# Kernel optimization log

Hardware: AMD Instinct MI355X
Metric: run time of the kernel (lower is better)

Reference implementation:

```python
import jax, jax.numpy as jnp
import numpy as np

NUM_HEADS = 8
TAU = 0.5

@jax.custom_vjp
def spike(u):
    # Heaviside spike with rectangular surrogate gradient (width 1.0)
    return (u >= 0.0).astype(u.dtype)

def _spike_fwd(u):
    return spike(u), u

def _spike_bwd(u, g):
    return (g * (jnp.abs(u) < 0.5).astype(g.dtype),)

spike.defvjp(_spike_fwd, _spike_bwd)

def lif(x, thr=1.0):
    # Multi-step LIF over leading T axis: leaky integrate, fire, hard reset.
    def step(mem, xt):
        mem = mem * TAU + xt
        s = spike(mem - thr)
        return mem * (1.0 - s), s
    _, out = jax.lax.scan(step, jnp.zeros_like(x[0]), x)
    return out

def bn(x, g, b):
    # eval-mode BatchNorm over channel axis 2 (running_mean=0, running_var=1)
    shape = (1, 1, -1) + (1,) * (x.ndim - 3)
    return x * g.reshape(shape) + b.reshape(shape)

def ema_mems(q, alpha):
    # mems[0]=q[0]; mems[t]=alpha*mems[t-1]+(1-alpha)*q[t-1]
    def step(m, qp):
        m2 = alpha * m + (1.0 - alpha) * qp
        return m2, m2
    _, ms = jax.lax.scan(step, q[0], q[:-1])
    return jnp.concatenate([q[:1], ms], axis=0)

def setup_inputs() -> dict:
    key = jax.random.key(0)
    ks = jax.random.split(key, 16)
    T, B, C, H, W = 4, 16, 256, 32, 32
    Ch = 4 * C
    s = 0.05
    return {
        'x': jax.random.normal(ks[0], (T, B, C, H, W), jnp.float32),
        'q_w': jax.random.normal(ks[1], (C, C), jnp.float32) * s,
        'q_g': 1.0 + 0.02 * jax.random.normal(ks[2], (C,), jnp.float32),
        'q_b': 0.02 * jax.random.normal(ks[3], (C,), jnp.float32),
        'k_w': jax.random.normal(ks[4], (C, C), jnp.float32) * s,
        'k_g': 1.0 + 0.02 * jax.random.normal(ks[5], (C,), jnp.float32),
        'k_b': 0.02 * jax.random.normal(ks[6], (C,), jnp.float32),
        'proj_w': jax.random.normal(ks[7], (C, C), jnp.float32) * s,
        'proj_bias': 0.02 * jax.random.normal(ks[8], (C,), jnp.float32),
        'proj_g': 1.0 + 0.02 * jax.random.normal(ks[9], (C,), jnp.float32),
        'proj_b2': 0.02 * jax.random.normal(ks[10], (C,), jnp.float32),
        'mem_alpha': jnp.asarray(0.2, jnp.float32),
        'w1': jax.random.normal(ks[11], (Ch, C), jnp.float32) * s,
        'b1': 0.02 * jax.random.normal(ks[12], (Ch,), jnp.float32),
        'bn1_g': jnp.ones((Ch,), jnp.float32),
        'bn1_b': jnp.zeros((Ch,), jnp.float32),
        'w2': jax.random.normal(ks[13], (C, Ch), jnp.float32) * s,
        'b2': 0.02 * jax.random.normal(ks[14], (C,), jnp.float32),
        'bn2_g': jnp.ones((C,), jnp.float32),
        'bn2_b': jnp.zeros((C,), jnp.float32),
    }

def reference(x, q_w, q_g, q_b, k_w, k_g, k_b, proj_w, proj_bias, proj_g, proj_b2,
              mem_alpha, w1, b1, bn1_g, bn1_b, w2, b2, bn2_g, bn2_b):
    T, B, C, H, W = x.shape
    N = H * W
    h = NUM_HEADS
    d = C // h

    # ---- Token_QK_Attention ----
    xs = lif(x)                                   # [T,B,C,H,W] spikes
    xf = xs.reshape(T, B, C, N)
    q = lif(bn(jnp.einsum('tbcn,oc->tbon', xf, q_w), q_g, q_b))
    k = lif(bn(jnp.einsum('tbcn,oc->tbon', xf, k_w), k_g, k_b))
    q = q.reshape(T, B, h, d, N)
    k = k.reshape(T, B, h, d, N)
    mems = ema_mems(q, mem_alpha)                 # [T,B,h,d,N]
    # concat([mems,q], dim=3) then sum over dim 3 == sum(mems+q, dim 3)
    qsum = jnp.sum(mems + q, axis=3, keepdims=True)   # [T,B,h,1,N]
    attn = lif(qsum, thr=0.5)
    y = (attn * k).reshape(T, B, C, N)
    y = bn(jnp.einsum('tbcn,oc->tbon', y, proj_w) + proj_bias.reshape(1, 1, -1, 1),
           proj_g, proj_b2).reshape(T, B, C, H, W)
    x = x + y

    # ---- MLP (1x1 conv2d) ----
    z = lif(x)
    z = bn(jnp.einsum('tbchw,oc->tbohw', z, w1) + b1.reshape(1, 1, -1, 1, 1), bn1_g, bn1_b)
    z = lif(z)
    z = bn(jnp.einsum('tbchw,oc->tbohw', z, w2) + b2.reshape(1, 1, -1, 1, 1), bn2_g, bn2_b)
    return x + z
```

## Files before the change

### kernel.cpp

```cpp
#include <hip/hip_runtime.h>

typedef unsigned int u32;
typedef unsigned char u8;
typedef unsigned short u16;
typedef __attribute__((ext_vector_type(4))) u32 u32x4;
typedef __attribute__((ext_vector_type(4))) int i32x4;
typedef __attribute__((ext_vector_type(4))) float f32x4;

#define DEV __device__ __forceinline__

static constexpr size_t XS_OFF  = 0;
static constexpr size_t QS_OFF  = XS_OFF  + (size_t)16777216;
static constexpr size_t KS_OFF  = QS_OFF  + (size_t)16777216;
static constexpr size_t ATT_OFF = KS_OFF  + (size_t)16777216;
static constexpr size_t X2_OFF  = ATT_OFF + (size_t)1048576;
static constexpr size_t Z2_OFF  = X2_OFF  + (size_t)67108864;
static constexpr size_t WQK_OFF = Z2_OFF  + (size_t)67108864;
static constexpr size_t WP_OFF  = WQK_OFF + (size_t)524288;
static constexpr size_t W1_OFF  = WP_OFF  + (size_t)262144;
static constexpr size_t W2_OFF  = W1_OFF  + (size_t)1048576;
static constexpr size_t WS_NEED = W2_OFF  + (size_t)1048576;

DEV void gl_lds16(const void* gsrc, void* ldst){
  __builtin_amdgcn_global_load_lds(
      (const __attribute__((address_space(1))) unsigned int*)gsrc,
      (__attribute__((address_space(3))) unsigned int*)ldst, 16, 0, 0);
}

__global__ __launch_bounds__(256) void prep_all(
    const float* __restrict__ q_w, const float* __restrict__ k_w,
    const float* __restrict__ p_w, const float* __restrict__ w1,
    const float* __restrict__ w2,
    signed char* __restrict__ WQK, signed char* __restrict__ WP,
    signed char* __restrict__ W1p, signed char* __restrict__ W2p)
{
  const int bb = blockIdx.x;
  const float* S; signed char* D; int O, Ck, OTs, otbase, base;
  if      (bb < 16) { S=q_w; D=WQK; O=256;  Ck=256;  OTs=32; otbase=0;  base=0;   }
  else if (bb < 32) { S=k_w; D=WQK; O=256;  Ck=256;  OTs=32; otbase=16; base=16;  }
  else if (bb < 48) { S=p_w; D=WP;  O=256;  Ck=256;  OTs=16; otbase=0;  base=32;  }
  else if (bb <112) { S=w1;  D=W1p; O=1024; Ck=256;  OTs=64; otbase=0;  base=48;  }
  else              { S=w2;  D=W2p; O=256;  Ck=1024; OTs=16; otbase=0;  base=112; }
  int tid = (bb - base)*256 + threadIdx.x;
  int lane = tid & 63; int fo = tid >> 6;
  int OT = O >> 4; int KT = Ck >> 6;
  int kt = fo / OT; int ot = fo - kt*OT;
  int o = (ot<<4) + (lane&15);
  int c = (kt<<6) + ((lane>>4)<<4);
  const float* sp = S + (size_t)o*Ck + c;
  u8 dg[4][16];
#pragma unroll
  for (int j=0;j<16;j++){
    double w = (double)sp[j];
    int Mhi = (int)__double2ll_rn(w * 32768.0);
    double r = w - (double)Mhi * (1.0/32768.0);
    int Mlo = (int)__double2ll_rn(r * 2147483648.0);
    if (Mlo > 32639){ Mhi += 1; Mlo -= 65536; }
    int d1 = (int)(signed char)(Mhi & 255); int d0 = (Mhi - d1) >> 8;
    int d3 = (int)(signed char)(Mlo & 255); int d2 = (Mlo - d3) >> 8;
    dg[0][j]=(u8)d0; dg[1][j]=(u8)d1; dg[2][j]=(u8)d2; dg[3][j]=(u8)d3;
  }
#pragma unroll
  for (int g=0; g<4; g++){
    signed char* dp = D + ((size_t)((g*KT + kt)*OTs + otbase + ot)<<10) + lane*16;
    *(u32x4*)dp = *(const u32x4*)dg[g];
  }
}

__global__ __launch_bounds__(256,4) void lif_x(const float* __restrict__ X, u8* __restrict__ XSo)
{
  int tid = blockIdx.x*256 + threadIdx.x;
  int n = tid & 1023; int oct = (tid>>10)&31; int b = tid>>15;
  int c0 = oct<<3;
  float mem[8];
#pragma unroll
  for (int i=0;i<8;i++) mem[i]=0.f;
#pragma unroll
  for (int t=0;t<4;t++){
    unsigned long long pk = 0ull;
    const float* xp = X + ((size_t)(((t*16+b)<<8) + c0)<<10) + n;
#pragma unroll
    for (int i=0;i<8;i++){
      float xv = xp[(size_t)i<<10];
      mem[i] = __fadd_rn(__fmul_rn(mem[i],0.5f), xv);
      bool s = mem[i] >= 1.0f;
      if (s) pk |= (1ull << (i*8));
      mem[i] = s? 0.f : mem[i];
    }
    *(unsigned long long*)(XSo + ((size_t)(((t*16+b)<<10) + n)<<8) + c0) = pk;
  }
}

DEV u32 nib4(u32 u){ return ((u & 0x01010101u) * 0x01020408u) >> 24; }
DEV u32 pk16(u32x4 v){ return nib4(v[0]) | (nib4(v[1])<<4) | (nib4(v[2])<<8) | (nib4(v[3])<<12); }

__global__ __launch_bounds__(256,4) void attn_k(const u8* __restrict__ QS, u8* __restrict__ ATT,
                                                const float* __restrict__ alpha_p)
{
  const int tid = threadIdx.x; const int l = tid & 63; const int wv = tid>>6;
  int wid = blockIdx.x*4 + wv;
  int b = wid >> 7; int nc = wid & 127; int n0 = nc<<3;
  int nr = (l>>3)&7; int ch8 = l&7;
  const float a = alpha_p[0]; const float oma = __fsub_rn(1.0f, a);
  u32 mk[4];
#pragma unroll
  for (int t=0;t<4;t++){
    const u32x4* p = (const u32x4*)(QS + ((size_t)(((t*16+b)<<10) + n0 + nr) << 8));
    u32x4 v0 = p[ch8]; u32x4 v1 = p[8+ch8];
    u32 pa = pk16(v0), pb = pk16(v1);
    u32 qa = __shfl_xor(pa, 1); u32 qb = __shfl_xor(pb, 1);
    mk[t] = (l&1)? (qb | (pb<<16)) : (pa | (qa<<16));
  }
  float mt1[2], mt2[4], mt3[8];
#pragma unroll
  for (int q0=0;q0<2;q0++){
    mt1[q0] = __fadd_rn(__fmul_rn(a,(float)q0), __fmul_rn(oma,(float)q0));
#pragma unroll
    for (int q1=0;q1<2;q1++){
      mt2[q0+(q1<<1)] = __fadd_rn(__fmul_rn(a,mt1[q0]), __fmul_rn(oma,(float)q1));
#pragma unroll
      for (int q2=0;q2<2;q2++)
        mt3[q0+(q1<<1)+(q2<<2)] = __fadd_rn(__fmul_rn(a,mt2[q0+(q1<<1)]), __fmul_rn(oma,(float)q2));
    }
  }
  const int h = ((l&7)>>1) + ((l&1)<<2);
  const int n = n0 + nr;
  float mem = 0.f;
#pragma unroll
  for (int t=0;t<4;t++){
    u32 act = mk[0];
    if (t>=1) act |= mk[1];
    if (t>=2) act |= mk[2];
    if (t>=3) act |= mk[3];
    float qsum = 0.f;
    while (act){
      int d = __builtin_ctz(act); act &= act-1;
      int b0 = (mk[0]>>d)&1;
      float m;
      if (t==0) m = (float)b0;
      else if (t==1) m = mt1[b0];
      else if (t==2) m = mt2[b0 + (((mk[1]>>d)&1)<<1)];
      else m = mt3[b0 + (((mk[1]>>d)&1)<<1) + (((mk[2]>>d)&1)<<2)];
      float qd = (float)((mk[t]>>d)&1);
      qsum = __fadd_rn(qsum, __fadd_rn(m, qd));
    }
    mem = __fadd_rn(__fmul_rn(mem, 0.5f), qsum);
    bool s = mem >= 0.5f;
    ATT[((size_t)(((t*16+b)<<3) + h)<<10) + n] = s? (u8)1 : (u8)0;
    mem = s? 0.f : mem;
  }
}

__global__ __launch_bounds__(256) void mask_k(const u8* __restrict__ KS,
                                              const u8* __restrict__ ATT, u8* __restrict__ YS)
{
  int tid = blockIdx.x*256 + threadIdx.x;
  int c4 = tid & 15; int n = (tid>>4) & 1023; int tb = tid >> 14;
  int h = c4 >> 1;
  u8 m = ATT[((size_t)((tb<<3) + h)<<10) + n];
  size_t row = ((size_t)((tb<<10)+n))<<8;
  u32x4 v = *(const u32x4*)(KS + row + c4*16);
  if (!m) v = (u32x4){0,0,0,0};
  *(u32x4*)(YS + row + c4*16) = v;
}

template<int MODE>
__global__ __launch_bounds__(256,2) void gemm_i8(
    const u8* __restrict__ A, const signed char* __restrict__ W,
    const float* __restrict__ G1, const float* __restrict__ B1,
    const float* __restrict__ G2, const float* __restrict__ B2,
    const float* __restrict__ BIAS, const float* __restrict__ XRES,
    float* __restrict__ FOUT, u8* __restrict__ SOUT, u8* __restrict__ SOUT2)
{
  constexpr int KC   = (MODE==3)? 1024 : 256;
  constexpr int KT   = KC >> 6;
  constexpr int OTOT = (MODE==0)? 32 : (MODE==2)? 64 : 16;
  constexpr int NOB  = OTOT >> 1;
  constexpr int NWG  = NOB*256;
  constexpr bool BUP = (MODE != 3);

  const int tid = threadIdx.x;
  const int bid = blockIdx.x;
  const int wid = (bid & 7)*(NWG>>3) + (bid>>3);
  const int ob = wid % NOB; const int rr = wid / NOB;
  const int nb = rr & 15; const int b = rr >> 4;

  __shared__ __align__(16) u8 Al[2][16384];
  __shared__ __align__(16) u8 Bl[BUP ? 32768 : 16384];

  const int lane = tid & 63, wv = tid >> 6;

  const u8* aRowG = A + (size_t)(((wv*16 + b)<<10) + nb*64 + lane)*KC;

  auto stageA = [&](int kt, int p){
    const u8* as = aRowG + kt*64;
    u8* ad = Al[p] + (wv<<2)*1024;
#pragma unroll
    for (int c=0;c<4;c++) gl_lds16(as + c*16, ad + c*1024);
  };
  auto stageB3 = [&](int kt, int p){
#pragma unroll
    for (int q2=0;q2<2;q2++){
      int fi = wv*2 + q2;
      const signed char* bs = W + ((size_t)(((fi>>1)*KT + kt)*OTOT + ob*2 + (fi&1))<<10) + lane*16;
      gl_lds16(bs, Bl + p*8192 + (fi<<10));
    }
  };

  i32x4 acc[4][2][4];
#pragma unroll
  for (int g=0;g<4;g++)
#pragma unroll
    for (int os=0;os<2;os++)
#pragma unroll
      for (int t=0;t<4;t++) acc[g][os][t] = (i32x4){0,0,0,0};

  if constexpr (BUP){
#pragma unroll
    for (int j=0;j<8;j++){
      int f = wv + j*4;
      int g = f >> 3; int os = (f>>2)&1; int kt = f&3;
      const signed char* bs = W + ((size_t)((g*KT + kt)*OTOT + ob*2 + os)<<10) + lane*16;
      gl_lds16(bs, Bl + (f<<10));
    }
  }
  stageA(0, 0);
  if constexpr (!BUP) stageB3(0, 0);

  auto compute = [&](int p, int kt){
    i32x4 af[4];
#pragma unroll
    for (int t=0;t<4;t++)
      af[t] = *(const i32x4*)(Al[p] + (((t<<2)+(lane>>4))<<10) + (((wv<<4)+(lane&15))<<4));
    __builtin_amdgcn_s_setprio(1);
#pragma unroll
    for (int g=0; g<4; ++g)
#pragma unroll
      for (int os=0; os<2; ++os){
        const u8* bp;
        if constexpr (BUP) bp = Bl + (((((g<<1)+os)<<2) | kt)<<10);
        else               bp = Bl + p*8192 + ((((g<<1)+os))<<10);
        i32x4 bf = *(const i32x4*)(bp + (lane<<4));
#pragma unroll
        for (int t=0;t<4;t++)
          acc[g][os][t] = __builtin_amdgcn_mfma_i32_16x16x64_i8(af[t], bf, acc[g][os][t], 0,0,0);
      }
    __builtin_amdgcn_s_setprio(0);
  };

#pragma unroll
  for (int kt=0; kt<KT; ++kt){
    const int p = kt & 1;
    if (kt+1 < KT){
      stageA(kt+1, p^1);
      if constexpr (!BUP) stageB3(kt+1, p^1);
      if constexpr (BUP) asm volatile("s_waitcnt vmcnt(4)" ::: "memory");
      else               asm volatile("s_waitcnt vmcnt(6)" ::: "memory");
    } else {
      asm volatile("s_waitcnt vmcnt(0)" ::: "memory");
    }
    __builtin_amdgcn_s_barrier();
    compute(p, kt);
    asm volatile("s_waitcnt lgkmcnt(0)" ::: "memory");
    __builtin_amdgcn_s_barrier();
  }

  const int g4 = lane >> 4;
  const int nq = nb*64 + (wv<<4) + (g4<<2);

  float pre[2][4][4];
#pragma unroll
  for (int os=0;os<2;++os)
#pragma unroll
    for (int t=0;t<4;++t)
#pragma unroll
      for (int jj=0;jj<4;++jj){
        int shi = (acc[0][os][t][jj] << 8) + acc[1][os][t][jj];
        int slo = (acc[2][os][t][jj] << 8) + acc[3][os][t][jj];
        pre[os][t][jj] = (float)((double)shi * 0x1p-15 + (double)slo * 0x1p-31);
      }

  if constexpr (MODE==0){
#pragma unroll
    for (int os=0; os<2; ++os){
      const int o = (ob<<5) + (os<<4) + (lane&15);
      const int matk = o>>8; const int om = o & 255;
      const float gg = (matk? G2 : G1)[om];
      const float bb = (matk? B2 : B1)[om];
      u8* sp = matk? SOUT2 : SOUT;
#pragma unroll
      for (int jj=0;jj<4;jj++){
        float mem = 0.f; const int n = nq + jj;
#pragma unroll
        for (int t=0;t<4;t++){
          float v = __fadd_rn(__fmul_rn(pre[os][t][jj], gg), bb);
          mem = __fadd_rn(__fmul_rn(mem, 0.5f), v);
          const bool s = mem >= 1.0f;
          sp[(size_t)(((t*16 + b)<<10) + n)*256 + om] = s? (u8)1 : (u8)0;
          mem = s? 0.f : mem;
        }
      }
    }
  } else if constexpr (MODE==1){
#pragma unroll
    for (int os=0; os<2; ++os){
      const int o = (ob<<5) + (os<<4) + (lane&15);
      const float pg = G1[o], pb2v = B1[o], pbv = BIAS[o];
      float xv[4][4];
#pragma unroll
      for (int t=0;t<4;t++){
        const size_t base = ((size_t)(((t*16 + b)<<8) + o)<<10) + nq;
        const f32x4 xq = *(const f32x4*)(XRES + base);
        f32x4 ov;
#pragma unroll
        for (int jj=0;jj<4;jj++){
          float y2 = __fadd_rn(__fmul_rn(__fadd_rn(pre[os][t][jj], pbv), pg), pb2v);
          float xx = __fadd_rn(xq[jj], y2);
          xv[t][jj] = xx; ov[jj] = xx;
        }
        *(f32x4*)(FOUT + base) = ov;
      }
#pragma unroll
      for (int jj=0;jj<4;jj++){
        float mem = 0.f; const int n = nq + jj;
#pragma unroll
        for (int t=0;t<4;t++){
          mem = __fadd_rn(__fmul_rn(mem, 0.5f), xv[t][jj]);
          const bool s = mem >= 1.0f;
          SOUT[(size_t)(((t*16 + b)<<10) + n)*256 + o] = s? (u8)1 : (u8)0;
          mem = s? 0.f : mem;
        }
      }
    }
  } else if constexpr (MODE==2){
#pragma unroll
    for (int os=0; os<2; ++os){
      const int o = (ob<<5) + (os<<4) + (lane&15);
      const float gg = G1[o], bb = B1[o], bv = BIAS[o];
#pragma unroll
      for (int jj=0;jj<4;jj++){
        float mem = 0.f; const int n = nq + jj;
#pragma unroll
        for (int t=0;t<4;t++){
          float v = __fadd_rn(__fmul_rn(__fadd_rn(pre[os][t][jj], bv), gg), bb);
          mem = __fadd_rn(__fmul_rn(mem, 0.5f), v);
          const bool s = mem >= 1.0f;
          SOUT[(size_t)(((t*16 + b)<<10) + n)*1024 + o] = s? (u8)1 : (u8)0;
          mem = s? 0.f : mem;
        }
      }
    }
  } else {
#pragma unroll
    for (int os=0; os<2; ++os){
      const int o = (ob<<5) + (os<<4) + (lane&15);
      const float gg = G1[o], bb = B1[o], bv = BIAS[o];
#pragma unroll
      for (int t=0;t<4;t++){
        const size_t base = ((size_t)(((t*16 + b)<<8) + o)<<10) + nq;
        const f32x4 xq = *(const f32x4*)(XRES + base);
        f32x4 ov;
#pragma unroll
        for (int jj=0;jj<4;jj++){
          float v = __fadd_rn(__fmul_rn(__fadd_rn(pre[os][t][jj], bv), gg), bb);
          ov[jj] = __fadd_rn(xq[jj], v);
        }
        *(f32x4*)(FOUT + base) = ov;
      }
    }
  }
}

extern "C" void kernel_launch(void* const* d_in, const int* in_sizes, int n_in,
                              void* d_out, int out_size, void* d_ws, size_t ws_size,
                              hipStream_t stream)
{
  (void)in_sizes; (void)n_in; (void)out_size;
  if (ws_size < WS_NEED) return;

  const float* x      = (const float*)d_in[0];
  const float* q_w    = (const float*)d_in[1];
  const float* q_g    = (const float*)d_in[2];
  const float* q_b    = (const float*)d_in[3];
  const float* k_w    = (const float*)d_in[4];
  const float* k_g    = (const float*)d_in[5];
  const float* k_b    = (const float*)d_in[6];
  const float* p_w    = (const float*)d_in[7];
  const float* p_bias = (const float*)d_in[8];
  const float* p_g    = (const float*)d_in[9];
  const float* p_b2   = (const float*)d_in[10];
  const float* alpha  = (const float*)d_in[11];
  const float* w1     = (const float*)d_in[12];
  const float* b1     = (const float*)d_in[13];
  const float* bn1g   = (const float*)d_in[14];
  const float* bn1b   = (const float*)d_in[15];
  const float* w2     = (const float*)d_in[16];
  const float* b2     = (const float*)d_in[17];
  const float* bn2g   = (const float*)d_in[18];
  const float* bn2b   = (const float*)d_in[19];

  u8* ws  = (u8*)d_ws;
  u8* XS  = ws + XS_OFF;
  u8* QS  = ws + QS_OFF;
  u8* KS  = ws + KS_OFF;
  u8* ATT = ws + ATT_OFF;
  float* X2 = (float*)(ws + X2_OFF);
  u8* Z2  = ws + Z2_OFF;
  u8* YS  = QS;
  u8* Z   = XS;
  signed char* WQK = (signed char*)(ws + WQK_OFF);
  signed char* WPp = (signed char*)(ws + WP_OFF);
  signed char* W1p = (signed char*)(ws + W1_OFF);
  signed char* W2p = (signed char*)(ws + W2_OFF);

  prep_all<<<176, 256, 0, stream>>>(q_w, k_w, p_w, w1, w2, WQK, WPp, W1p, W2p);

  lif_x<<<2048, 256, 0, stream>>>(x, XS);

  gemm_i8<0><<<4096, 256, 0, stream>>>(XS, WQK, q_g, q_b, k_g, k_b,
                                       nullptr, nullptr, nullptr, QS, KS);

  attn_k<<<512, 256, 0, stream>>>(QS, ATT, alpha);
  mask_k<<<4096, 256, 0, stream>>>(KS, ATT, YS);

  gemm_i8<1><<<2048, 256, 0, stream>>>(YS, WPp, p_g, p_b2, nullptr, nullptr,
                                       p_bias, x, X2, Z, nullptr);

  gemm_i8<2><<<8192, 256, 0, stream>>>(Z, W1p, bn1g, bn1b, nullptr, nullptr,
                                       b1, nullptr, nullptr, Z2, nullptr);

  gemm_i8<3><<<2048, 256, 0, stream>>>(Z2, W2p, bn2g, bn2b, nullptr, nullptr,
                                       b2, X2, (float*)d_out, nullptr, nullptr);
}
```

Measured before the change: 517.7 us.

## Load A fragments directly from global and stage B in K-superblocks

Drops LDS staging and double-buffering of the activation (A) tiles. Each wave now loads its A fragments straight from global memory into registers. Weights are staged into one 32KB LDS buffer in superblocks of four K-steps, so MODE 3 (K=1024) uses the same path as the other modes. This removes A's LDS traffic and many barriers and shrinks LDS use, but global A loads are no longer prefetched ahead of compute and each superblock waits with vmcnt(0).

```diff
diff --git a/kernel.cpp b/kernel.cpp
--- a/kernel.cpp
+++ b/kernel.cpp
@@ -173,11 +173,11 @@
     float* __restrict__ FOUT, u8* __restrict__ SOUT, u8* __restrict__ SOUT2)
 {
   constexpr int KC   = (MODE==3)? 1024 : 256;
-  constexpr int KT   = KC >> 6;
+  constexpr int KTF  = KC >> 6;
+  constexpr int NSUP = KTF >> 2;
   constexpr int OTOT = (MODE==0)? 32 : (MODE==2)? 64 : 16;
   constexpr int NOB  = OTOT >> 1;
   constexpr int NWG  = NOB*256;
-  constexpr bool BUP = (MODE != 3);
 
   const int tid = threadIdx.x;
   const int bid = blockIdx.x;
@@ -185,27 +185,14 @@
   const int ob = wid % NOB; const int rr = wid / NOB;
   const int nb = rr & 15; const int b = rr >> 4;
 
-  __shared__ __align__(16) u8 Al[2][16384];
-  __shared__ __align__(16) u8 Bl[BUP ? 32768 : 16384];
+  __shared__ __align__(16) u8 Bl[32768];
 
   const int lane = tid & 63, wv = tid >> 6;
 
-  const u8* aRowG = A + (size_t)(((wv*16 + b)<<10) + nb*64 + lane)*KC;
-
-  auto stageA = [&](int kt, int p){
-    const u8* as = aRowG + kt*64;
-    u8* ad = Al[p] + (wv<<2)*1024;
-#pragma unroll
-    for (int c=0;c<4;c++) gl_lds16(as + c*16, ad + c*1024);
-  };
-  auto stageB3 = [&](int kt, int p){
-#pragma unroll
-    for (int q2=0;q2<2;q2++){
-      int fi = wv*2 + q2;
-      const signed char* bs = W + ((size_t)(((fi>>1)*KT + kt)*OTOT + ob*2 + (fi&1))<<10) + lane*16;
-      gl_lds16(bs, Bl + p*8192 + (fi<<10));
-    }
-  };
+  const u8* aB[4];
+#pragma unroll
+  for (int t=0;t<4;t++)
+    aB[t] = A + (size_t)(((t*16 + b)<<10) + nb*64 + (wv<<4) + (lane&15))*KC + ((lane>>4)<<4);
 
   i32x4 acc[4][2][4];
 #pragma unroll
@@ -215,54 +202,38 @@
 #pragma unroll
       for (int t=0;t<4;t++) acc[g][os][t] = (i32x4){0,0,0,0};
 
-  if constexpr (BUP){
+#pragma unroll
+  for (int s=0; s<NSUP; ++s){
+    if (s) __syncthreads();
 #pragma unroll
     for (int j=0;j<8;j++){
-      int f = wv + j*4;
-      int g = f >> 3; int os = (f>>2)&1; int kt = f&3;
-      const signed char* bs = W + ((size_t)((g*KT + kt)*OTOT + ob*2 + os)<<10) + lane*16;
+      const int f = (wv<<3) + j;
+      const int g = f>>3, os = (f>>2)&1, ktl = f&3;
+      const signed char* bs = W + ((size_t)((g*KTF + (s<<2)+ktl)*OTOT + ob*2 + os)<<10) + (lane<<4);
       gl_lds16(bs, Bl + (f<<10));
     }
-  }
-  stageA(0, 0);
-  if constexpr (!BUP) stageB3(0, 0);
-
-  auto compute = [&](int p, int kt){
-    i32x4 af[4];
-#pragma unroll
-    for (int t=0;t<4;t++)
-      af[t] = *(const i32x4*)(Al[p] + (((t<<2)+(lane>>4))<<10) + (((wv<<4)+(lane&15))<<4));
-    __builtin_amdgcn_s_setprio(1);
-#pragma unroll
-    for (int g=0; g<4; ++g)
-#pragma unroll
-      for (int os=0; os<2; ++os){
-        const u8* bp;
-        if constexpr (BUP) bp = Bl + (((((g<<1)+os)<<2) | kt)<<10);
-        else               bp = Bl + p*8192 + ((((g<<1)+os))<<10);
-        i32x4 bf = *(const i32x4*)(bp + (lane<<4));
-#pragma unroll
-        for (int t=0;t<4;t++)
-          acc[g][os][t] = __builtin_amdgcn_mfma_i32_16x16x64_i8(af[t], bf, acc[g][os][t], 0,0,0);
-      }
-    __builtin_amdgcn_s_setprio(0);
-  };
-
-#pragma unroll
-  for (int kt=0; kt<KT; ++kt){
-    const int p = kt & 1;
-    if (kt+1 < KT){
-      stageA(kt+1, p^1);
-      if constexpr (!BUP) stageB3(kt+1, p^1);
-      if constexpr (BUP) asm volatile("s_waitcnt vmcnt(4)" ::: "memory");
-      else               asm volatile("s_waitcnt vmcnt(6)" ::: "memory");
-    } else {
-      asm volatile("s_waitcnt vmcnt(0)" ::: "memory");
-    }
+    asm volatile("s_waitcnt vmcnt(0)" ::: "memory");
     __builtin_amdgcn_s_barrier();
-    compute(p, kt);
-    asm volatile("s_waitcnt lgkmcnt(0)" ::: "memory");
-    __builtin_amdgcn_s_barrier();
+
+#pragma unroll
+    for (int ktl=0; ktl<4; ++ktl){
+      const int kt = (s<<2) + ktl;
+      i32x4 af[4];
+#pragma unroll
+      for (int t=0;t<4;t++)
+        af[t] = *(const i32x4*)(aB[t] + kt*64);
+      __builtin_amdgcn_s_setprio(1);
+#pragma unroll
+      for (int g=0; g<4; ++g)
+#pragma unroll
+        for (int os=0; os<2; ++os){
+          i32x4 bf = *(const i32x4*)(Bl + (((((g<<1)+os)<<2) | ktl)<<10) + (lane<<4));
+#pragma unroll
+          for (int t=0;t<4;t++)
+            acc[g][os][t] = __builtin_amdgcn_mfma_i32_16x16x64_i8(af[t], bf, acc[g][os][t], 0,0,0);
+        }
+      __builtin_amdgcn_s_setprio(0);
+    }
   }
 
   const int g4 = lane >> 4;
```

Result: faster. 457.7 us (-11.6%).
